# Kernel optimization log

Hardware: AMD Instinct MI355X
Metric: run time of the kernel (lower is better)

## Reference

```python
import jax, jax.numpy as jnp
import numpy as np

FS = 48000.0
B, N = 16, 96000


def _rbj_low_shelf(fc, gain_db, Q):
    A = 10.0 ** (gain_db / 40.0)
    w0 = 2.0 * jnp.pi * fc / FS
    alpha = jnp.sin(w0) / (2.0 * Q)
    cosw = jnp.cos(w0)
    sqrtA = jnp.sqrt(A)
    b0 = A * (A + 1.0 - (A - 1.0) * cosw + 2.0 * sqrtA * alpha)
    b1 = 2.0 * A * (A - 1.0 - (A + 1.0) * cosw)
    b2 = A * (A + 1.0 - (A - 1.0) * cosw - 2.0 * sqrtA * alpha)
    a0 = A + 1.0 + (A - 1.0) * cosw + 2.0 * sqrtA * alpha
    a1 = -2.0 * (A - 1.0 + (A + 1.0) * cosw)
    a2 = A + 1.0 + (A - 1.0) * cosw - 2.0 * sqrtA * alpha
    return jnp.stack([b0, b1, b2, a1, a2], axis=-1) / a0[..., None]


def _rbj_high_shelf(fc, gain_db, Q):
    A = 10.0 ** (gain_db / 40.0)
    w0 = 2.0 * jnp.pi * fc / FS
    alpha = jnp.sin(w0) / (2.0 * Q)
    cosw = jnp.cos(w0)
    sqrtA = jnp.sqrt(A)
    b0 = A * (A + 1.0 + (A - 1.0) * cosw + 2.0 * sqrtA * alpha)
    b1 = -2.0 * A * (A - 1.0 + (A + 1.0) * cosw)
    b2 = A * (A + 1.0 + (A - 1.0) * cosw - 2.0 * sqrtA * alpha)
    a0 = A + 1.0 - (A - 1.0) * cosw + 2.0 * sqrtA * alpha
    a1 = 2.0 * (A - 1.0 - (A + 1.0) * cosw)
    a2 = A + 1.0 - (A - 1.0) * cosw - 2.0 * sqrtA * alpha
    return jnp.stack([b0, b1, b2, a1, a2], axis=-1) / a0[..., None]


def _rbj_peaking(fc, gain_db, Q):
    A = 10.0 ** (gain_db / 40.0)
    w0 = 2.0 * jnp.pi * fc / FS
    alpha = jnp.sin(w0) / (2.0 * Q)
    cosw = jnp.cos(w0)
    b0 = 1.0 + alpha * A
    b1 = -2.0 * cosw
    b2 = 1.0 - alpha * A
    a0 = 1.0 + alpha / A
    a1 = -2.0 * cosw
    a2 = 1.0 - alpha / A
    return jnp.stack([b0, b1, b2, a1, a2], axis=-1) / a0[..., None]


def setup_inputs() -> dict:
    key = jax.random.key(0)
    ks = jax.random.split(key, 6)
    x = jax.random.normal(ks[0], (B, N), dtype=jnp.float32) * 0.5
    low_gain_db = jax.random.normal(ks[1], (B, N), dtype=jnp.float32) * 4.0
    mid_gain_db = jax.random.normal(ks[2], (B, N), dtype=jnp.float32) * 4.0
    # mid_fc in [50, 8000] Hz, mid_Q in [0.2, 4.0] (ranges enforced by clamp in forward)
    mid_fc = 50.0 + jax.random.uniform(ks[3], (B, N), dtype=jnp.float32) * 7950.0
    mid_Q = 0.2 + jax.random.uniform(ks[4], (B, N), dtype=jnp.float32) * 3.8
    high_gain_db = jax.random.normal(ks[5], (B, N), dtype=jnp.float32) * 4.0
    return {"x": x, "low_gain_db": low_gain_db, "mid_gain_db": mid_gain_db,
            "mid_fc": mid_fc, "mid_Q": mid_Q, "high_gain_db": high_gain_db}


def _biquad(xn, z1, z2, c):
    # c: (..., 5) = [b0, b1, b2, a1, a2]
    b0, b1, b2, a1, a2 = c[..., 0], c[..., 1], c[..., 2], c[..., 3], c[..., 4]
    yn = b0 * xn + z1
    z1n = b1 * xn - a1 * yn + z2
    z2n = b2 * xn - a2 * yn
    return yn, z1n, z2n


def _tonestack(x, low_gain_db, mid_gain_db, mid_fc, mid_Q, high_gain_db):
    mid_fc = jnp.clip(mid_fc, 50.0, 8000.0)
    mid_Q = jnp.clip(mid_Q, 0.2, 4.0)
    # Per-sample time-varying coefficients, each (B, N, 5)
    cl = _rbj_low_shelf(jnp.float32(120.0), low_gain_db, jnp.float32(0.707))
    cm = _rbj_peaking(mid_fc, mid_gain_db, mid_Q)
    ch = _rbj_high_shelf(jnp.float32(4000.0), high_gain_db, jnp.float32(0.707))

    def step(z, inp):
        xn, cln, cmn, chn = inp  # xn: (B,), c*: (B, 5)
        z1l, z2l, z1m, z2m, z1h, z2h = z
        yl, z1l, z2l = _biquad(xn, z1l, z2l, cln)
        ym, z1m, z2m = _biquad(yl, z1m, z2m, cmn)
        yh, z1h, z2h = _biquad(ym, z1h, z2h, chn)
        return (z1l, z2l, z1m, z2m, z1h, z2h), yh

    z0 = tuple(jnp.zeros((x.shape[0],), x.dtype) for _ in range(6))
    xs = (x.T, cl.transpose(1, 0, 2), cm.transpose(1, 0, 2), ch.transpose(1, 0, 2))
    _, ys = jax.lax.scan(step, z0, xs)  # ys: (N, B)
    return ys.T


def reference(x, low_gain_db, mid_gain_db, mid_fc, mid_Q, high_gain_db):
    return _tonestack(x, low_gain_db, mid_gain_db, mid_fc, mid_Q, high_gain_db)
```

## Files before the change

### kernel.cpp

```cpp
#include <hip/hip_runtime.h>


static constexpr int B   = 16;
static constexpr int N   = 96000;
static constexpr int L   = 12;
static constexpr int C   = 8000;
static constexpr int NC  = B * C;
static constexpr int GP  = 125;
static constexpr int BGP = B * GP;

#define FS_INV (1.0f / 48000.0f)

__device__ __forceinline__ float frcp(float x) { return __builtin_amdgcn_rcpf(x); }

struct Coefs {
  float b0l, b1l, b2l, a1l, a2l;
  float b0m, b1m, b2m, a1m, a2m;
  float b0h, b1h, b2h, a1h, a2h;
};

__device__ __forceinline__ Coefs make_coefs(float gl, float gm, float fcm,
                                            float qm, float gh) {
  Coefs o;
  const float K = 0.08304820237218406f;
  {
    const float cw = 0.9998766325f;
    const float al = 0.0111084287f;
    float A  = __builtin_amdgcn_exp2f(gl * K);
    float sA = __builtin_amdgcn_sqrtf(A);
    float Ap1 = A + 1.0f, Am1 = A - 1.0f;
    float t = Am1 * cw, u = 2.0f * sA * al;
    float b0 = A * (Ap1 - t + u);
    float b1 = 2.0f * A * (Am1 - Ap1 * cw);
    float b2 = A * (Ap1 - t - u);
    float a0 = Ap1 + t + u;
    float a1 = -2.0f * (Am1 + Ap1 * cw);
    float a2 = Ap1 + t - u;
    float r = frcp(a0);
    o.b0l = b0 * r; o.b1l = b1 * r; o.b2l = b2 * r; o.a1l = a1 * r; o.a2l = a2 * r;
  }
  {
    float fc = fminf(fmaxf(fcm, 50.0f), 8000.0f);
    float Q  = fminf(fmaxf(qm, 0.2f), 4.0f);
    float rev = fc * FS_INV;
    float sw  = __builtin_amdgcn_sinf(rev);
    float cwm = __builtin_amdgcn_cosf(rev);
    float A   = __builtin_amdgcn_exp2f(gm * K);
    float iA  = frcp(A);
    float alpha = sw * 0.5f * frcp(Q);
    float aA = alpha * A, aiA = alpha * iA;
    float b0 = 1.0f + aA, b1 = -2.0f * cwm, b2 = 1.0f - aA;
    float a0 = 1.0f + aiA, a2 = 1.0f - aiA;
    float r = frcp(a0);
    float b1r = b1 * r;
    o.b0m = b0 * r; o.b1m = b1r; o.b2m = b2 * r; o.a1m = b1r; o.a2m = a2 * r;
  }
  {
    const float cw = 0.8660254038f;
    const float al = 0.3536067893f;
    float A  = __builtin_amdgcn_exp2f(gh * K);
    float sA = __builtin_amdgcn_sqrtf(A);
    float Ap1 = A + 1.0f, Am1 = A - 1.0f;
    float t = Am1 * cw, u = 2.0f * sA * al;
    float b0 = A * (Ap1 + t + u);
    float b1 = -2.0f * A * (Am1 + Ap1 * cw);
    float b2 = A * (Ap1 + t - u);
    float a0 = Ap1 - t + u;
    float a1 = 2.0f * (Am1 - Ap1 * cw);
    float a2 = Ap1 - t - u;
    float r = frcp(a0);
    o.b0h = b0 * r; o.b1h = b1 * r; o.b2h = b2 * r; o.a1h = a1 * r; o.a2h = a2 * r;
  }
  return o;
}

__device__ __forceinline__ float stepF(float v[6], float xc, const Coefs& k) {
  float yl = fmaf(k.b0l, xc, v[0]);
  float n0 = fmaf(k.b1l, xc, fmaf(-k.a1l, yl, v[1]));
  float n1 = fmaf(k.b2l, xc, -k.a2l * yl);
  float ym = fmaf(k.b0m, yl, v[2]);
  float n2 = fmaf(k.b1m, yl, fmaf(-k.a1m, ym, v[3]));
  float n3 = fmaf(k.b2m, yl, -k.a2m * ym);
  float yh = fmaf(k.b0h, ym, v[4]);
  float n4 = fmaf(k.b1h, ym, fmaf(-k.a1h, yh, v[5]));
  float n5 = fmaf(k.b2h, ym, -k.a2h * yh);
  v[0] = n0; v[1] = n1; v[2] = n2; v[3] = n3; v[4] = n4; v[5] = n5;
  return yh;
}
__device__ __forceinline__ void stepF0(float v[6], const Coefs& k) {
  float yl = v[0];
  float n0 = fmaf(-k.a1l, yl, v[1]);
  float n1 = -k.a2l * yl;
  float ym = fmaf(k.b0m, yl, v[2]);
  float n2 = fmaf(k.b1m, yl, fmaf(-k.a1m, ym, v[3]));
  float n3 = fmaf(k.b2m, yl, -k.a2m * ym);
  float yh = fmaf(k.b0h, ym, v[4]);
  float n4 = fmaf(k.b1h, ym, fmaf(-k.a1h, yh, v[5]));
  float n5 = fmaf(k.b2h, ym, -k.a2h * yh);
  v[0] = n0; v[1] = n1; v[2] = n2; v[3] = n3; v[4] = n4; v[5] = n5;
}
__device__ __forceinline__ void stepM(float v[4], const Coefs& k) {
  float ym = v[0];
  float n0 = fmaf(-k.a1m, ym, v[1]);
  float n1 = -k.a2m * ym;
  float yh = fmaf(k.b0h, ym, v[2]);
  float n2 = fmaf(k.b1h, ym, fmaf(-k.a1h, yh, v[3]));
  float n3 = fmaf(k.b2h, ym, -k.a2h * yh);
  v[0] = n0; v[1] = n1; v[2] = n2; v[3] = n3;
}
__device__ __forceinline__ void stepH(float v[2], const Coefs& k) {
  float yh = v[0];
  float n0 = fmaf(-k.a1h, yh, v[1]);
  float n1 = -k.a2h * yh;
  v[0] = n0; v[1] = n1;
}

struct Aff {
  float c0[6], c1[6];
  float c2[4], c3[4];
  float c4[2], c5[2];
  float d[6];
};

__device__ __forceinline__ void loadAff(const float* __restrict__ p, Aff& a) {
  const float4* q = reinterpret_cast<const float4*>(p);
  float4 f0 = q[0], f1 = q[1], f2 = q[2], f3 = q[3];
  float4 f4 = q[4], f5 = q[5], f6 = q[6], f7 = q[7];
  a.c0[0] = f0.x; a.c0[1] = f0.y; a.c0[2] = f0.z; a.c0[3] = f0.w;
  a.c0[4] = f1.x; a.c0[5] = f1.y;
  a.c1[0] = f1.z; a.c1[1] = f1.w; a.c1[2] = f2.x; a.c1[3] = f2.y;
  a.c1[4] = f2.z; a.c1[5] = f2.w;
  a.c2[0] = f3.x; a.c2[1] = f3.y; a.c2[2] = f3.z; a.c2[3] = f3.w;
  a.c3[0] = f4.x; a.c3[1] = f4.y; a.c3[2] = f4.z; a.c3[3] = f4.w;
  a.c4[0] = f5.x; a.c4[1] = f5.y; a.c5[0] = f5.z; a.c5[1] = f5.w;
  a.d[0] = f6.x; a.d[1] = f6.y; a.d[2] = f6.z; a.d[3] = f6.w;
  a.d[4] = f7.x; a.d[5] = f7.y;
}

__device__ __forceinline__ void storeAff(float* __restrict__ p, const Aff& a) {
  float4* q = reinterpret_cast<float4*>(p);
  q[0] = make_float4(a.c0[0], a.c0[1], a.c0[2], a.c0[3]);
  q[1] = make_float4(a.c0[4], a.c0[5], a.c1[0], a.c1[1]);
  q[2] = make_float4(a.c1[2], a.c1[3], a.c1[4], a.c1[5]);
  q[3] = make_float4(a.c2[0], a.c2[1], a.c2[2], a.c2[3]);
  q[4] = make_float4(a.c3[0], a.c3[1], a.c3[2], a.c3[3]);
  q[5] = make_float4(a.c4[0], a.c4[1], a.c5[0], a.c5[1]);
  q[6] = make_float4(a.d[0], a.d[1], a.d[2], a.d[3]);
  q[7] = make_float4(a.d[4], a.d[5], 0.f, 0.f);
}

__device__ __forceinline__ void applyM6(const Aff& A, const float v[6], float r[6]) {
  r[0] = v[0]*A.c0[0] + v[1]*A.c1[0];
  r[1] = v[0]*A.c0[1] + v[1]*A.c1[1];
  r[2] = v[0]*A.c0[2] + v[1]*A.c1[2] + v[2]*A.c2[0] + v[3]*A.c3[0];
  r[3] = v[0]*A.c0[3] + v[1]*A.c1[3] + v[2]*A.c2[1] + v[3]*A.c3[1];
  r[4] = v[0]*A.c0[4] + v[1]*A.c1[4] + v[2]*A.c2[2] + v[3]*A.c3[2]
       + v[4]*A.c4[0] + v[5]*A.c5[0];
  r[5] = v[0]*A.c0[5] + v[1]*A.c1[5] + v[2]*A.c2[3] + v[3]*A.c3[3]
       + v[4]*A.c4[1] + v[5]*A.c5[1];
}
__device__ __forceinline__ void applyAff(const Aff& A, const float s[6], float r[6]) {
  float t[6];
  applyM6(A, s, t);
  #pragma unroll
  for (int i = 0; i < 6; ++i) r[i] = t[i] + A.d[i];
}

__device__ __forceinline__ void composeInto(const Aff& Mc, const Aff& acc, Aff& R) {
  applyM6(Mc, acc.c0, R.c0);
  applyM6(Mc, acc.c1, R.c1);
  {
    const float* a = acc.c2; float* r = R.c2;
    r[0] = a[0]*Mc.c2[0] + a[1]*Mc.c3[0];
    r[1] = a[0]*Mc.c2[1] + a[1]*Mc.c3[1];
    r[2] = a[0]*Mc.c2[2] + a[1]*Mc.c3[2] + a[2]*Mc.c4[0] + a[3]*Mc.c5[0];
    r[3] = a[0]*Mc.c2[3] + a[1]*Mc.c3[3] + a[2]*Mc.c4[1] + a[3]*Mc.c5[1];
  }
  {
    const float* a = acc.c3; float* r = R.c3;
    r[0] = a[0]*Mc.c2[0] + a[1]*Mc.c3[0];
    r[1] = a[0]*Mc.c2[1] + a[1]*Mc.c3[1];
    r[2] = a[0]*Mc.c2[2] + a[1]*Mc.c3[2] + a[2]*Mc.c4[0] + a[3]*Mc.c5[0];
    r[3] = a[0]*Mc.c2[3] + a[1]*Mc.c3[3] + a[2]*Mc.c4[1] + a[3]*Mc.c5[1];
  }
  {
    const float* a = acc.c4; float* r = R.c4;
    r[0] = a[0]*Mc.c4[0] + a[1]*Mc.c5[0];
    r[1] = a[0]*Mc.c4[1] + a[1]*Mc.c5[1];
  }
  {
    const float* a = acc.c5; float* r = R.c5;
    r[0] = a[0]*Mc.c4[0] + a[1]*Mc.c5[0];
    r[1] = a[0]*Mc.c4[1] + a[1]*Mc.c5[1];
  }
  float t[6];
  applyM6(Mc, acc.d, t);
  #pragma unroll
  for (int i = 0; i < 6; ++i) R.d[i] = t[i] + Mc.d[i];
}

__device__ __forceinline__ void setIdentity(Aff& a) {
  #pragma unroll
  for (int i = 0; i < 6; ++i) { a.c0[i] = 0.f; a.c1[i] = 0.f; a.d[i] = 0.f; }
  #pragma unroll
  for (int i = 0; i < 4; ++i) { a.c2[i] = 0.f; a.c3[i] = 0.f; }
  a.c4[0] = 0.f; a.c4[1] = 0.f; a.c5[0] = 0.f; a.c5[1] = 0.f;
  a.c0[0] = 1.f; a.c1[1] = 1.f; a.c2[0] = 1.f; a.c3[1] = 1.f;
  a.c4[0] = 1.f; a.c5[1] = 1.f;
}

__device__ __forceinline__ Aff shflUpAff(const Aff& a, int d) {
  Aff r;
  #pragma unroll
  for (int i = 0; i < 6; ++i) {
    r.c0[i] = __shfl_up(a.c0[i], d);
    r.c1[i] = __shfl_up(a.c1[i], d);
    r.d[i]  = __shfl_up(a.d[i],  d);
  }
  #pragma unroll
  for (int i = 0; i < 4; ++i) {
    r.c2[i] = __shfl_up(a.c2[i], d);
    r.c3[i] = __shfl_up(a.c3[i], d);
  }
  r.c4[0] = __shfl_up(a.c4[0], d); r.c4[1] = __shfl_up(a.c4[1], d);
  r.c5[0] = __shfl_up(a.c5[0], d); r.c5[1] = __shfl_up(a.c5[1], d);
  return r;
}

__global__ __launch_bounds__(256) void k_phaseA(
    const float* __restrict__ x,  const float* __restrict__ lg,
    const float* __restrict__ mg, const float* __restrict__ fc,
    const float* __restrict__ qq, const float* __restrict__ hg,
    float* __restrict__ comp, float* __restrict__ gtot) {
  int id = blockIdx.x * 256 + threadIdx.x;
  int lane = threadIdx.x & 63;
  int b = id / C, c = id % C;
  const int base = b * N + c * L;

  float c0[6] = {1.f, 0.f, 0.f, 0.f, 0.f, 0.f};
  float c1[6] = {0.f, 1.f, 0.f, 0.f, 0.f, 0.f};
  float c2[4] = {1.f, 0.f, 0.f, 0.f};
  float c3[4] = {0.f, 1.f, 0.f, 0.f};
  float c4[2] = {1.f, 0.f};
  float c5[2] = {0.f, 1.f};
  float dd[6] = {0.f, 0.f, 0.f, 0.f, 0.f, 0.f};

  #pragma unroll
  for (int i = 0; i < L; i += 4) {
    float4 xv = *reinterpret_cast<const float4*>(x  + base + i);
    float4 lv = *reinterpret_cast<const float4*>(lg + base + i);
    float4 mv = *reinterpret_cast<const float4*>(mg + base + i);
    float4 fv = *reinterpret_cast<const float4*>(fc + base + i);
    float4 qv = *reinterpret_cast<const float4*>(qq + base + i);
    float4 hv = *reinterpret_cast<const float4*>(hg + base + i);
    const float* xp = &xv.x; const float* lp = &lv.x; const float* mp = &mv.x;
    const float* fp = &fv.x; const float* qp = &qv.x; const float* hp = &hv.x;
    #pragma unroll
    for (int j = 0; j < 4; ++j) {
      Coefs k = make_coefs(lp[j], mp[j], fp[j], qp[j], hp[j]);
      stepF0(c0, k);
      stepF0(c1, k);
      stepM(c2, k);
      stepM(c3, k);
      stepH(c4, k);
      stepH(c5, k);
      stepF(dd, xp[j], k);
    }
  }

  Aff a;
  #pragma unroll
  for (int i = 0; i < 6; ++i) { a.c0[i] = c0[i]; a.c1[i] = c1[i]; a.d[i] = dd[i]; }
  #pragma unroll
  for (int i = 0; i < 4; ++i) { a.c2[i] = c2[i]; a.c3[i] = c3[i]; }
  a.c4[0] = c4[0]; a.c4[1] = c4[1]; a.c5[0] = c5[0]; a.c5[1] = c5[1];

  #pragma unroll
  for (int dlt = 1; dlt < 64; dlt <<= 1) {
    Aff o = shflUpAff(a, dlt);
    if (lane >= dlt) { Aff r; composeInto(a, o, r); a = r; }
  }

  storeAff(comp + (size_t)id * 32, a);
  if (lane == 63) {
    int g = c >> 6;
    storeAff(gtot + (size_t)(b * GP + g) * 32, a);
  }
}

__global__ __launch_bounds__(64) void k_phaseB(const float* __restrict__ gtot,
                                               float* __restrict__ gstart) {
  int b = blockIdx.x, lane = threadIdx.x;
  float s[6] = {0.f, 0.f, 0.f, 0.f, 0.f, 0.f};

  for (int r = 0; r < 2; ++r) {
    int g = r * 64 + lane;
    Aff a;
    if (g < GP) loadAff(gtot + (size_t)(b * GP + g) * 32, a);
    else        setIdentity(a);
    #pragma unroll
    for (int dlt = 1; dlt < 64; dlt <<= 1) {
      Aff o = shflUpAff(a, dlt);
      if (lane >= dlt) { Aff t; composeInto(a, o, t); a = t; }
    }
    float e[6];
    applyAff(a, s, e);
    float st[6];
    #pragma unroll
    for (int i = 0; i < 6; ++i) {
      float p = __shfl_up(e[i], 1);
      st[i] = (lane == 0) ? s[i] : p;
    }
    if (g < GP) {
      float* o = gstart + (size_t)(b * GP + g) * 8;
      float4* ov = reinterpret_cast<float4*>(o);
      ov[0] = make_float4(st[0], st[1], st[2], st[3]);
      ov[1] = make_float4(st[4], st[5], 0.f, 0.f);
    }
    #pragma unroll
    for (int i = 0; i < 6; ++i) s[i] = __shfl(e[i], 63);
  }
}

__global__ __launch_bounds__(256) void k_phaseC(
    const float* __restrict__ x,  const float* __restrict__ lg,
    const float* __restrict__ mg, const float* __restrict__ fc,
    const float* __restrict__ qq, const float* __restrict__ hg,
    const float* __restrict__ comp, const float* __restrict__ gstart,
    float* __restrict__ y) {
  int id = blockIdx.x * 256 + threadIdx.x;
  int b = id / C, c = id % C;
  int p = c & 63, g = c >> 6;
  const int base = b * N + c * L;

  const float4* gs = reinterpret_cast<const float4*>(gstart + (size_t)(b * GP + g) * 8);
  float4 g0 = gs[0], g1 = gs[1];
  float sg[6] = {g0.x, g0.y, g0.z, g0.w, g1.x, g1.y};

  float z[6];
  if (p == 0) {
    #pragma unroll
    for (int i = 0; i < 6; ++i) z[i] = sg[i];
  } else {
    Aff P;
    loadAff(comp + (size_t)(id - 1) * 32, P);
    applyAff(P, sg, z);
  }

  #pragma unroll
  for (int i = 0; i < L; i += 4) {
    float4 xv = *reinterpret_cast<const float4*>(x  + base + i);
    float4 lv = *reinterpret_cast<const float4*>(lg + base + i);
    float4 mv = *reinterpret_cast<const float4*>(mg + base + i);
    float4 fv = *reinterpret_cast<const float4*>(fc + base + i);
    float4 qv = *reinterpret_cast<const float4*>(qq + base + i);
    float4 hv = *reinterpret_cast<const float4*>(hg + base + i);
    const float* xp = &xv.x; const float* lp = &lv.x; const float* mp = &mv.x;
    const float* fp = &fv.x; const float* qp = &qv.x; const float* hp = &hv.x;
    float4 outv;
    float* op = &outv.x;
    #pragma unroll
    for (int j = 0; j < 4; ++j) {
      Coefs k = make_coefs(lp[j], mp[j], fp[j], qp[j], hp[j]);
      op[j] = stepF(z, xp[j], k);
    }
    *reinterpret_cast<float4*>(y + base + i) = outv;
  }
}

__global__ void k_naive(const float* __restrict__ x,  const float* __restrict__ lg,
                        const float* __restrict__ mg, const float* __restrict__ fc,
                        const float* __restrict__ qq, const float* __restrict__ hg,
                        float* __restrict__ y) {
  int b = threadIdx.x;
  if (b >= B) return;
  float z[6] = {0.f, 0.f, 0.f, 0.f, 0.f, 0.f};
  for (int n = 0; n < N; ++n) {
    int i = b * N + n;
    Coefs k = make_coefs(lg[i], mg[i], fc[i], qq[i], hg[i]);
    y[i] = stepF(z, x[i], k);
  }
}

extern "C" void kernel_launch(void* const* d_in, const int* in_sizes, int n_in,
                              void* d_out, int out_size, void* d_ws, size_t ws_size,
                              hipStream_t stream) {
  const float* x  = (const float*)d_in[0];
  const float* lg = (const float*)d_in[1];
  const float* mg = (const float*)d_in[2];
  const float* fc = (const float*)d_in[3];
  const float* qq = (const float*)d_in[4];
  const float* hg = (const float*)d_in[5];
  float* y = (float*)d_out;

  size_t need = ((size_t)NC * 32 + (size_t)BGP * 32 + (size_t)BGP * 8) * sizeof(float);
  if (ws_size < need) {
    k_naive<<<1, 64, 0, stream>>>(x, lg, mg, fc, qq, hg, y);
    return;
  }
  float* comp   = (float*)d_ws;
  float* gtot   = comp + (size_t)NC * 32;
  float* gstart = gtot + (size_t)BGP * 32;

  k_phaseA<<<NC / 256, 256, 0, stream>>>(x, lg, mg, fc, qq, hg, comp, gtot);
  k_phaseB<<<B, 64, 0, stream>>>(gtot, gstart);
  k_phaseC<<<NC / 256, 256, 0, stream>>>(x, lg, mg, fc, qq, hg, comp, gstart, y);
}
```

Measured before the change: 120.7 us.

## Recompute per-thread prefix maps in phase C instead of storing them

Phase A no longer writes each thread's 32-float prefix affine map to global memory. Phase C rebuilds the local map and redoes the wave scan, so each thread gets its predecessor's prefix by shuffle. This removes a large workspace write and read. The chunk length is halved to 6 samples, doubling thread count and the number of group partials that phase B scans. Occupancy hints are added to the launch bounds. In exchange, phase C redoes the map construction and the shuffle scan, which costs more ALU work.

```diff
diff --git a/kernel.cpp b/kernel.cpp
--- a/kernel.cpp
+++ b/kernel.cpp
@@ -3,11 +3,11 @@
 
 static constexpr int B   = 16;
 static constexpr int N   = 96000;
-static constexpr int L   = 12;
-static constexpr int C   = 8000;
+static constexpr int L   = 6;
+static constexpr int C   = 16000;
 static constexpr int NC  = B * C;
-static constexpr int GP  = 125;
-static constexpr int BGP = B * GP;
+static constexpr int GPR = 250;
+static constexpr int BGP = B * GPR;
 
 #define FS_INV (1.0f / 48000.0f)
 
@@ -227,16 +227,23 @@
   return r;
 }
 
-__global__ __launch_bounds__(256) void k_phaseA(
-    const float* __restrict__ x,  const float* __restrict__ lg,
-    const float* __restrict__ mg, const float* __restrict__ fc,
-    const float* __restrict__ qq, const float* __restrict__ hg,
-    float* __restrict__ comp, float* __restrict__ gtot) {
-  int id = blockIdx.x * 256 + threadIdx.x;
-  int lane = threadIdx.x & 63;
-  int b = id / C, c = id % C;
-  const int base = b * N + c * L;
-
+__device__ __forceinline__ void waveScanAff(Aff& a, int lane) {
+  #pragma unroll
+  for (int dlt = 1; dlt < 64; dlt <<= 1) {
+    Aff o = shflUpAff(a, dlt);
+    if (lane >= dlt) { Aff r; composeInto(a, o, r); a = r; }
+  }
+}
+
+__device__ __forceinline__ void load6(const float* __restrict__ p, float v[6]) {
+  const float2* q = reinterpret_cast<const float2*>(p);
+  float2 a = q[0], b = q[1], c = q[2];
+  v[0] = a.x; v[1] = a.y; v[2] = b.x; v[3] = b.y; v[4] = c.x; v[5] = c.y;
+}
+
+__device__ __forceinline__ void buildMap(
+    const float xs[6], const float ls[6], const float ms[6],
+    const float fs[6], const float qs[6], const float hs[6], Aff& a) {
   float c0[6] = {1.f, 0.f, 0.f, 0.f, 0.f, 0.f};
   float c1[6] = {0.f, 1.f, 0.f, 0.f, 0.f, 0.f};
   float c2[4] = {1.f, 0.f, 0.f, 0.f};
@@ -244,47 +251,49 @@
   float c4[2] = {1.f, 0.f};
   float c5[2] = {0.f, 1.f};
   float dd[6] = {0.f, 0.f, 0.f, 0.f, 0.f, 0.f};
-
-  #pragma unroll
-  for (int i = 0; i < L; i += 4) {
-    float4 xv = *reinterpret_cast<const float4*>(x  + base + i);
-    float4 lv = *reinterpret_cast<const float4*>(lg + base + i);
-    float4 mv = *reinterpret_cast<const float4*>(mg + base + i);
-    float4 fv = *reinterpret_cast<const float4*>(fc + base + i);
-    float4 qv = *reinterpret_cast<const float4*>(qq + base + i);
-    float4 hv = *reinterpret_cast<const float4*>(hg + base + i);
-    const float* xp = &xv.x; const float* lp = &lv.x; const float* mp = &mv.x;
-    const float* fp = &fv.x; const float* qp = &qv.x; const float* hp = &hv.x;
-    #pragma unroll
-    for (int j = 0; j < 4; ++j) {
-      Coefs k = make_coefs(lp[j], mp[j], fp[j], qp[j], hp[j]);
-      stepF0(c0, k);
-      stepF0(c1, k);
-      stepM(c2, k);
-      stepM(c3, k);
-      stepH(c4, k);
-      stepH(c5, k);
-      stepF(dd, xp[j], k);
-    }
-  }
-
-  Aff a;
+  #pragma unroll
+  for (int j = 0; j < L; ++j) {
+    Coefs k = make_coefs(ls[j], ms[j], fs[j], qs[j], hs[j]);
+    stepF0(c0, k);
+    stepF0(c1, k);
+    stepM(c2, k);
+    stepM(c3, k);
+    stepH(c4, k);
+    stepH(c5, k);
+    stepF(dd, xs[j], k);
+  }
   #pragma unroll
   for (int i = 0; i < 6; ++i) { a.c0[i] = c0[i]; a.c1[i] = c1[i]; a.d[i] = dd[i]; }
   #pragma unroll
   for (int i = 0; i < 4; ++i) { a.c2[i] = c2[i]; a.c3[i] = c3[i]; }
   a.c4[0] = c4[0]; a.c4[1] = c4[1]; a.c5[0] = c5[0]; a.c5[1] = c5[1];
-
-  #pragma unroll
-  for (int dlt = 1; dlt < 64; dlt <<= 1) {
-    Aff o = shflUpAff(a, dlt);
-    if (lane >= dlt) { Aff r; composeInto(a, o, r); a = r; }
-  }
-
-  storeAff(comp + (size_t)id * 32, a);
+}
+
+__global__ __launch_bounds__(256, 4) void k_phaseA(
+    const float* __restrict__ x,  const float* __restrict__ lg,
+    const float* __restrict__ mg, const float* __restrict__ fc,
+    const float* __restrict__ qq, const float* __restrict__ hg,
+    float* __restrict__ gtot) {
+  int id = blockIdx.x * 256 + threadIdx.x;
+  int lane = threadIdx.x & 63;
+  int b = id / C, c = id % C;
+  const int base = b * N + c * L;
+
+  float xs[6], ls[6], ms[6], fs[6], qs[6], hs[6];
+  load6(x  + base, xs);
+  load6(lg + base, ls);
+  load6(mg + base, ms);
+  load6(fc + base, fs);
+  load6(qq + base, qs);
+  load6(hg + base, hs);
+
+  Aff a;
+  buildMap(xs, ls, ms, fs, qs, hs, a);
+  waveScanAff(a, lane);
+
   if (lane == 63) {
     int g = c >> 6;
-    storeAff(gtot + (size_t)(b * GP + g) * 32, a);
+    storeAff(gtot + (size_t)(b * GPR + g) * 32, a);
   }
 }
 
@@ -293,16 +302,12 @@
   int b = blockIdx.x, lane = threadIdx.x;
   float s[6] = {0.f, 0.f, 0.f, 0.f, 0.f, 0.f};
 
-  for (int r = 0; r < 2; ++r) {
+  for (int r = 0; r < (GPR + 63) / 64; ++r) {
     int g = r * 64 + lane;
     Aff a;
-    if (g < GP) loadAff(gtot + (size_t)(b * GP + g) * 32, a);
-    else        setIdentity(a);
-    #pragma unroll
-    for (int dlt = 1; dlt < 64; dlt <<= 1) {
-      Aff o = shflUpAff(a, dlt);
-      if (lane >= dlt) { Aff t; composeInto(a, o, t); a = t; }
-    }
+    if (g < GPR) loadAff(gtot + (size_t)(b * GPR + g) * 32, a);
+    else         setIdentity(a);
+    waveScanAff(a, lane);
     float e[6];
     applyAff(a, s, e);
     float st[6];
@@ -311,8 +316,8 @@
       float p = __shfl_up(e[i], 1);
       st[i] = (lane == 0) ? s[i] : p;
     }
-    if (g < GP) {
-      float* o = gstart + (size_t)(b * GP + g) * 8;
+    if (g < GPR) {
+      float* o = gstart + (size_t)(b * GPR + g) * 8;
       float4* ov = reinterpret_cast<float4*>(o);
       ov[0] = make_float4(st[0], st[1], st[2], st[3]);
       ov[1] = make_float4(st[4], st[5], 0.f, 0.f);
@@ -322,49 +327,60 @@
   }
 }
 
-__global__ __launch_bounds__(256) void k_phaseC(
+__global__ __launch_bounds__(256, 4) void k_phaseC(
     const float* __restrict__ x,  const float* __restrict__ lg,
     const float* __restrict__ mg, const float* __restrict__ fc,
     const float* __restrict__ qq, const float* __restrict__ hg,
-    const float* __restrict__ comp, const float* __restrict__ gstart,
-    float* __restrict__ y) {
+    const float* __restrict__ gstart, float* __restrict__ y) {
   int id = blockIdx.x * 256 + threadIdx.x;
+  int lane = threadIdx.x & 63;
   int b = id / C, c = id % C;
-  int p = c & 63, g = c >> 6;
+  int g = c >> 6;
   const int base = b * N + c * L;
 
-  const float4* gs = reinterpret_cast<const float4*>(gstart + (size_t)(b * GP + g) * 8);
-  float4 g0 = gs[0], g1 = gs[1];
-  float sg[6] = {g0.x, g0.y, g0.z, g0.w, g1.x, g1.y};
-
-  float z[6];
-  if (p == 0) {
+  {
+    float xs[6], ls[6], ms[6], fs[6], qs[6], hs[6];
+    load6(x  + base, xs);
+    load6(lg + base, ls);
+    load6(mg + base, ms);
+    load6(fc + base, fs);
+    load6(qq + base, qs);
+    load6(hg + base, hs);
+    Aff a;
+    buildMap(xs, ls, ms, fs, qs, hs, a);
+    waveScanAff(a, lane);
+
+    Aff e = shflUpAff(a, 1);
+
+    const float4* gs = reinterpret_cast<const float4*>(gstart + (size_t)(b * GPR + g) * 8);
+    float4 g0 = gs[0], g1 = gs[1];
+    float sg[6] = {g0.x, g0.y, g0.z, g0.w, g1.x, g1.y};
+
+    float z[6];
+    if (lane == 0) {
+      #pragma unroll
+      for (int i = 0; i < 6; ++i) z[i] = sg[i];
+    } else {
+      applyAff(e, sg, z);
+    }
+
+    float xs2[6], ls2[6], ms2[6], fs2[6], qs2[6], hs2[6];
+    load6(x  + base, xs2);
+    load6(lg + base, ls2);
+    load6(mg + base, ms2);
+    load6(fc + base, fs2);
+    load6(qq + base, qs2);
+    load6(hg + base, hs2);
+    float out[6];
     #pragma unroll
-    for (int i = 0; i < 6; ++i) z[i] = sg[i];
-  } else {
-    Aff P;
-    loadAff(comp + (size_t)(id - 1) * 32, P);
-    applyAff(P, sg, z);
-  }
-
-  #pragma unroll
-  for (int i = 0; i < L; i += 4) {
-    float4 xv = *reinterpret_cast<const float4*>(x  + base + i);
-    float4 lv = *reinterpret_cast<const float4*>(lg + base + i);
-    float4 mv = *reinterpret_cast<const float4*>(mg + base + i);
-    float4 fv = *reinterpret_cast<const float4*>(fc + base + i);
-    float4 qv = *reinterpret_cast<const float4*>(qq + base + i);
-    float4 hv = *reinterpret_cast<const float4*>(hg + base + i);
-    const float* xp = &xv.x; const float* lp = &lv.x; const float* mp = &mv.x;
-    const float* fp = &fv.x; const float* qp = &qv.x; const float* hp = &hv.x;
-    float4 outv;
-    float* op = &outv.x;
-    #pragma unroll
-    for (int j = 0; j < 4; ++j) {
-      Coefs k = make_coefs(lp[j], mp[j], fp[j], qp[j], hp[j]);
-      op[j] = stepF(z, xp[j], k);
+    for (int j = 0; j < L; ++j) {
+      Coefs k = make_coefs(ls2[j], ms2[j], fs2[j], qs2[j], hs2[j]);
+      out[j] = stepF(z, xs2[j], k);
     }
-    *reinterpret_cast<float4*>(y + base + i) = outv;
+    float2* yo = reinterpret_cast<float2*>(y + base);
+    yo[0] = make_float2(out[0], out[1]);
+    yo[1] = make_float2(out[2], out[3]);
+    yo[2] = make_float2(out[4], out[5]);
   }
 }
 
@@ -393,16 +409,15 @@
   const float* hg = (const float*)d_in[5];
   float* y = (float*)d_out;
 
-  size_t need = ((size_t)NC * 32 + (size_t)BGP * 32 + (size_t)BGP * 8) * sizeof(float);
+  size_t need = ((size_t)BGP * 32 + (size_t)BGP * 8) * sizeof(float);
   if (ws_size < need) {
     k_naive<<<1, 64, 0, stream>>>(x, lg, mg, fc, qq, hg, y);
     return;
   }
-  float* comp   = (float*)d_ws;
-  float* gtot   = comp + (size_t)NC * 32;
+  float* gtot   = (float*)d_ws;
   float* gstart = gtot + (size_t)BGP * 32;
 
-  k_phaseA<<<NC / 256, 256, 0, stream>>>(x, lg, mg, fc, qq, hg, comp, gtot);
+  k_phaseA<<<NC / 256, 256, 0, stream>>>(x, lg, mg, fc, qq, hg, gtot);
   k_phaseB<<<B, 64, 0, stream>>>(gtot, gstart);
-  k_phaseC<<<NC / 256, 256, 0, stream>>>(x, lg, mg, fc, qq, hg, comp, gstart, y);
-}
+  k_phaseC<<<NC / 256, 256, 0, stream>>>(x, lg, mg, fc, qq, hg, gstart, y);
+}
```

Measured after the change: 153.0 us. 1.27x slower.
